# Performance work log

Measured on AMD Instinct MI355X. Metric: run time of the kernel, lower is better.

The kernel has to match this reference:

```python
import jax, jax.numpy as jnp
import numpy as np

NUM_QUANTIZERS = 8


def setup_inputs() -> dict:
    key = jax.random.key(0)
    k1, k2 = jax.random.split(key)
    B, W, C = 16, 2048, 512
    Q, K = NUM_QUANTIZERS, 1024
    x = jax.random.normal(k1, (B, W, C), dtype=jnp.float32)
    # per-stage codebooks (shared_codebook=False), xavier-normal-ish scale
    codebooks = jax.random.normal(k2, (Q, K, C), dtype=jnp.float32) * (2.0 / (K + C)) ** 0.5
    return {"x": x, "codebooks": codebooks}


def reference(x, codebooks):
    """Residual quantization: per-stage cdist+argmin+lookup+residual update.

    x: [B, W, C] encoder latents; codebooks: [Q, K, C].
    Returns (final_z_q [B*W, C], commitment_loss scalar) — final_z_q is
    sum over quantizer stages of the straight-through quantized outputs
    (is_train=True path).
    """
    B, W, C = x.shape
    first_z_e = x.reshape(B * W, C)            # (b w) c
    z_e = first_z_e
    z_d = jnp.zeros_like(first_z_e)
    quant_sum = jnp.zeros_like(first_z_e)
    q_latent = jnp.float32(0.0)
    e_latent = jnp.float32(0.0)
    rq_latent = jnp.float32(0.0)
    for i in range(codebooks.shape[0]):
        cb = codebooks[i]                      # [K, C]
        # squared euclidean distances (argmin-equivalent to torch.cdist)
        dist2 = (jnp.sum(z_e * z_e, axis=1, keepdims=True)
                 - 2.0 * (z_e @ cb.T)
                 + jnp.sum(cb * cb, axis=1))   # [N, K]
        idx = jnp.argmin(dist2, axis=1)        # [N]
        z_q = cb[idx]                          # codebook lookup, [N, C]
        z_d = z_d + jax.lax.stop_gradient(z_q)
        q_latent = q_latent + jnp.mean((jax.lax.stop_gradient(z_e) - z_q) ** 2)
        e_latent = e_latent + jnp.mean((z_e - jax.lax.stop_gradient(z_q)) ** 2)
        rq_latent = rq_latent + jnp.mean((first_z_e - z_d) ** 2)
        # straight-through estimator (is_train=True)
        z_q_st = z_e + jax.lax.stop_gradient(z_q - z_e)
        quant_sum = quant_sum + z_q_st
        z_e = z_e - z_q_st
    commitment_loss = 0.75 * q_latent + e_latent + rq_latent
    return quant_sum, commitment_loss
```

## Files before the change

kernel.cpp:

```cpp
#include <hip/hip_runtime.h>

#define N_ROWS 32768
#define C_DIM  512
#define K_CODES 1024
#define Q_STAGES 8

typedef __attribute__((ext_vector_type(8))) short bf16x8;
typedef __attribute__((ext_vector_type(4))) float f32x4;
typedef __attribute__((ext_vector_type(4))) unsigned short u16x4;
typedef __attribute__((ext_vector_type(8))) unsigned short u16x8;

#define ZEH_OFF 0ull
#define ZEL_OFF 33554432ull
#define CBH_OFF 67108864ull
#define CBL_OFF 68157440ull
#define C2_OFF  69206016ull
#define IDX_OFF 69238784ull
#define RPT_OFF 69304320ull

#define GLD(gp, lp) __builtin_amdgcn_global_load_lds( \
    (const __attribute__((address_space(1))) void*)(gp), \
    (__attribute__((address_space(3))) void*)(lp), 16, 0, 0)

__device__ __forceinline__ float bf_hi_f(float f) {
    return __uint_as_float(__float_as_uint(f) & 0xFFFF0000u);
}
__device__ __forceinline__ unsigned short bf_hi_u(float f) {
    return (unsigned short)(__float_as_uint(f) >> 16);
}
__device__ __forceinline__ float u2f(unsigned short u) {
    return __uint_as_float(((unsigned int)u) << 16);
}

__global__ __launch_bounds__(256) void split_kernel(
    const float* __restrict__ src, unsigned short* __restrict__ h,
    unsigned short* __restrict__ l, int n4)
{
    int i = blockIdx.x * 256 + threadIdx.x;
    if (i >= n4) return;
    float4 v = *(const float4*)(src + (size_t)i * 4);
    u16x4 hv, lv;
    float f, hf;
    f = v.x; hv[0] = bf_hi_u(f); hf = bf_hi_f(f); lv[0] = bf_hi_u(f - hf);
    f = v.y; hv[1] = bf_hi_u(f); hf = bf_hi_f(f); lv[1] = bf_hi_u(f - hf);
    f = v.z; hv[2] = bf_hi_u(f); hf = bf_hi_f(f); lv[2] = bf_hi_u(f - hf);
    f = v.w; hv[3] = bf_hi_u(f); hf = bf_hi_f(f); lv[3] = bf_hi_u(f - hf);
    *(u16x4*)(h + (size_t)i * 4) = hv;
    *(u16x4*)(l + (size_t)i * 4) = lv;
}

__global__ __launch_bounds__(256) void rowsq_kernel(
    const float* __restrict__ src, float* __restrict__ dst, int nrows)
{
    int wave = (blockIdx.x * blockDim.x + threadIdx.x) >> 6;
    int lane = threadIdx.x & 63;
    if (wave >= nrows) return;
    const float* p = src + (size_t)wave * C_DIM + lane * 8;
    float4 a = *(const float4*)p;
    float4 b = *(const float4*)(p + 4);
    float s = a.x*a.x + a.y*a.y + a.z*a.z + a.w*a.w
            + b.x*b.x + b.y*b.y + b.z*b.z + b.w*b.w;
    #pragma unroll
    for (int off = 1; off < 64; off <<= 1) s += __shfl_xor(s, off);
    if (lane == 0) dst[wave] = s;
}

#define DBM2 128
#define DBNC 256
#define DBK 32
#define NSTEPS 64

__global__ __launch_bounds__(512, 2) void dist_kernel(
    const unsigned short* __restrict__ zeh, const unsigned short* __restrict__ zel,
    const unsigned short* __restrict__ cbh, const unsigned short* __restrict__ cbl,
    const float* __restrict__ c2s, unsigned short* __restrict__ idx_out)
{
    __shared__ unsigned short sA[3][2][DBM2 * DBK];
    __shared__ unsigned short sB[3][2][DBNC * DBK];
    __shared__ float c2_lds[K_CODES];

    const int tid  = threadIdx.x;
    const int lane = tid & 63;
    const int w    = tid >> 6;
    const int wr   = w >> 2;
    const int wc   = w & 3;
    const int lr   = lane & 15;
    const int kg   = lane >> 4;
    const int row0 = blockIdx.x * DBM2;

    for (int i = tid; i < K_CODES; i += 512) c2_lds[i] = c2s[i];

    const int srow = lane >> 2;
    const int scol = (((lane & 3) ^ ((srow >> 1) & 3))) * 8;
    const int aslot = (kg ^ ((lr >> 1) & 3)) * 8;

    float rbv[4][4];
    int   rbi[4][4];
    #pragma unroll
    for (int i = 0; i < 4; ++i)
        #pragma unroll
        for (int r = 0; r < 4; ++r) { rbv[i][r] = 3.4e38f; rbi[i][r] = 0x7fffffff; }

    f32x4 acc[4][4];
    #pragma unroll
    for (int i = 0; i < 4; ++i)
        #pragma unroll
        for (int j = 0; j < 4; ++j) acc[i][j] = (f32x4)0.f;

    auto stage = [&](int t, int b) {
        const int col0 = (t >> 4) * DBNC;
        const int kk = (t & 15) * DBK;
        GLD(zeh + (size_t)(row0 + w * 16 + srow) * C_DIM + kk + scol,
            &sA[b][0][(w * 16) * DBK]);
        GLD(zel + (size_t)(row0 + w * 16 + srow) * C_DIM + kk + scol,
            &sA[b][1][(w * 16) * DBK]);
        #pragma unroll
        for (int u = 0; u < 2; ++u) {
            const int rB = w * 32 + u * 16;
            GLD(cbh + (size_t)(col0 + rB + srow) * C_DIM + kk + scol,
                &sB[b][0][rB * DBK]);
            GLD(cbl + (size_t)(col0 + rB + srow) * C_DIM + kk + scol,
                &sB[b][1][rB * DBK]);
        }
    };

    __syncthreads();
    stage(0, 0);
    stage(1, 1);
    asm volatile("s_waitcnt vmcnt(6)" ::: "memory");
    __builtin_amdgcn_s_barrier();

    bf16x8 ah[4], al[4], bh[4], bl[4];
    #pragma unroll
    for (int mi = 0; mi < 4; ++mi)
        ah[mi] = *(const bf16x8*)&sA[0][0][(wr * 64 + mi * 16 + lr) * DBK + aslot];
    #pragma unroll
    for (int ni = 0; ni < 4; ++ni)
        bh[ni] = *(const bf16x8*)&sB[0][0][(wc * 64 + ni * 16 + lr) * DBK + aslot];

    int cur = 0;
    #pragma unroll 1
    for (int t = 0; t < NSTEPS; ++t) {
        const int nxt = (cur == 2) ? 0 : cur + 1;
        const int n2  = (nxt == 2) ? 0 : nxt + 1;

        asm volatile("s_waitcnt lgkmcnt(0)" ::: "memory");
        __builtin_amdgcn_sched_barrier(0);
        #pragma unroll
        for (int ni = 0; ni < 4; ++ni)
            bl[ni] = *(const bf16x8*)&sB[cur][1][(wc * 64 + ni * 16 + lr) * DBK + aslot];
        __builtin_amdgcn_sched_barrier(0);
        __builtin_amdgcn_s_setprio(1);
        #pragma unroll
        for (int mi = 0; mi < 4; ++mi)
            #pragma unroll
            for (int ni = 0; ni < 4; ++ni)
                acc[mi][ni] = __builtin_amdgcn_mfma_f32_16x16x32_bf16(
                    ah[mi], bh[ni], acc[mi][ni], 0, 0, 0);
        __builtin_amdgcn_s_setprio(0);
        __builtin_amdgcn_sched_barrier(0);
        __builtin_amdgcn_s_barrier();

        asm volatile("s_waitcnt lgkmcnt(0)" ::: "memory");
        __builtin_amdgcn_sched_barrier(0);
        #pragma unroll
        for (int mi = 0; mi < 4; ++mi)
            al[mi] = *(const bf16x8*)&sA[cur][1][(wr * 64 + mi * 16 + lr) * DBK + aslot];
        if (t < NSTEPS - 2) stage(t + 2, n2);
        if (t <= NSTEPS - 3) {
            asm volatile("s_waitcnt vmcnt(6)" ::: "memory");
        } else {
            asm volatile("s_waitcnt vmcnt(0)" ::: "memory");
        }
        __builtin_amdgcn_sched_barrier(0);
        __builtin_amdgcn_s_setprio(1);
        #pragma unroll
        for (int mi = 0; mi < 4; ++mi)
            #pragma unroll
            for (int ni = 0; ni < 4; ++ni)
                acc[mi][ni] = __builtin_amdgcn_mfma_f32_16x16x32_bf16(
                    ah[mi], bl[ni], acc[mi][ni], 0, 0, 0);
        __builtin_amdgcn_s_setprio(0);
        __builtin_amdgcn_sched_barrier(0);
        __builtin_amdgcn_s_barrier();

        asm volatile("s_waitcnt lgkmcnt(0)" ::: "memory");
        __builtin_amdgcn_sched_barrier(0);
        __builtin_amdgcn_s_setprio(1);
        #pragma unroll
        for (int mi = 0; mi < 4; ++mi)
            #pragma unroll
            for (int ni = 0; ni < 4; ++ni)
                acc[mi][ni] = __builtin_amdgcn_mfma_f32_16x16x32_bf16(
                    al[mi], bh[ni], acc[mi][ni], 0, 0, 0);
        __builtin_amdgcn_s_setprio(0);
        __builtin_amdgcn_sched_barrier(0);
        if (t < NSTEPS - 1) {
            #pragma unroll
            for (int mi = 0; mi < 4; ++mi)
                ah[mi] = *(const bf16x8*)&sA[nxt][0][(wr * 64 + mi * 16 + lr) * DBK + aslot];
            #pragma unroll
            for (int ni = 0; ni < 4; ++ni)
                bh[ni] = *(const bf16x8*)&sB[nxt][0][(wc * 64 + ni * 16 + lr) * DBK + aslot];
        }
        if ((t & 15) == 15) {
            const int col0 = (t >> 4) * DBNC;
            #pragma unroll
            for (int ni = 0; ni < 4; ++ni) {
                const int code = col0 + wc * 64 + ni * 16 + lr;
                const float c2v = c2_lds[code];
                #pragma unroll
                for (int mi = 0; mi < 4; ++mi)
                    #pragma unroll
                    for (int r = 0; r < 4; ++r) {
                        float d = fmaf(-2.f, acc[mi][ni][r], c2v);
                        if (d < rbv[mi][r]) { rbv[mi][r] = d; rbi[mi][r] = code; }
                    }
            }
            #pragma unroll
            for (int i = 0; i < 4; ++i)
                #pragma unroll
                for (int j = 0; j < 4; ++j) acc[i][j] = (f32x4)0.f;
        }
        __builtin_amdgcn_s_barrier();
        cur = nxt;
    }

    #pragma unroll
    for (int off = 1; off < 16; off <<= 1) {
        #pragma unroll
        for (int mi = 0; mi < 4; ++mi)
            #pragma unroll
            for (int r = 0; r < 4; ++r) {
                float ov = __shfl_xor(rbv[mi][r], off);
                int   oi = __shfl_xor(rbi[mi][r], off);
                if (ov < rbv[mi][r] || (ov == rbv[mi][r] && oi < rbi[mi][r])) {
                    rbv[mi][r] = ov; rbi[mi][r] = oi;
                }
            }
    }

    __syncthreads();
    float (*s_v)[4] = (float (*)[4])&sA[0][0][0];
    int   (*s_i)[4] = (int (*)[4])((char*)&sA[0][0][0] + DBM2 * 4 * 4);
    if (lr == 0) {
        #pragma unroll
        for (int mi = 0; mi < 4; ++mi)
            #pragma unroll
            for (int r = 0; r < 4; ++r) {
                int lrow = wr * 64 + mi * 16 + kg * 4 + r;
                s_v[lrow][wc] = rbv[mi][r];
                s_i[lrow][wc] = rbi[mi][r];
            }
    }
    __syncthreads();
    if (tid < DBM2) {
        float bv = s_v[tid][0]; int bi = s_i[tid][0];
        #pragma unroll
        for (int c = 1; c < 4; ++c) {
            float v = s_v[tid][c]; int i = s_i[tid][c];
            if (v < bv || (v == bv && i < bi)) { bv = v; bi = i; }
        }
        idx_out[row0 + tid] = (unsigned short)bi;
    }
}

__global__ __launch_bounds__(1024) void update_kernel(
    const int s, const float* __restrict__ x, const float* __restrict__ cb,
    const float* __restrict__ cb_next, const unsigned short* __restrict__ idx_sel,
    float* __restrict__ out, unsigned short* __restrict__ zeh,
    unsigned short* __restrict__ zel, unsigned short* __restrict__ cbh,
    unsigned short* __restrict__ cbl, float* __restrict__ rpart)
{
    if (blockIdx.x >= 2048) {
        int i = (blockIdx.x - 2048) * 1024 + threadIdx.x;
        float4 v = *(const float4*)(cb_next + (size_t)i * 4);
        u16x4 hv, lv;
        float f, hf;
        f = v.x; hv[0] = bf_hi_u(f); hf = bf_hi_f(f); lv[0] = bf_hi_u(f - hf);
        f = v.y; hv[1] = bf_hi_u(f); hf = bf_hi_f(f); lv[1] = bf_hi_u(f - hf);
        f = v.z; hv[2] = bf_hi_u(f); hf = bf_hi_f(f); lv[2] = bf_hi_u(f - hf);
        f = v.w; hv[3] = bf_hi_u(f); hf = bf_hi_f(f); lv[3] = bf_hi_u(f - hf);
        *(u16x4*)(cbh + (size_t)i * 4) = hv;
        *(u16x4*)(cbl + (size_t)i * 4) = lv;
        return;
    }

    __shared__ float swsum[16];
    const int wid = threadIdx.x >> 6, lane = threadIdx.x & 63;
    const int r = blockIdx.x * 16 + wid;
    const int bi = idx_sel[r];
    const size_t base = (size_t)r * C_DIM + lane * 8;
    const float* q = cb + (size_t)bi * C_DIM + lane * 8;

    float4 q0 = *(const float4*)q;
    float4 q1 = *(const float4*)(q + 4);
    float qq[8] = {q0.x, q0.y, q0.z, q0.w, q1.x, q1.y, q1.z, q1.w};

    float v[8];
    if (s == 0) {
        float4 z0 = *(const float4*)(x + base);
        float4 z1 = *(const float4*)(x + base + 4);
        v[0]=z0.x; v[1]=z0.y; v[2]=z0.z; v[3]=z0.w;
        v[4]=z1.x; v[5]=z1.y; v[6]=z1.z; v[7]=z1.w;
    } else {
        u16x8 h = *(const u16x8*)(zeh + base);
        u16x8 l = *(const u16x8*)(zel + base);
        #pragma unroll
        for (int j = 0; j < 8; ++j) v[j] = u2f(h[j]) + u2f(l[j]);
    }

    float rr[8];
    #pragma unroll
    for (int j = 0; j < 8; ++j) rr[j] = v[j] - qq[j];

    if (s < Q_STAGES - 1) {
        u16x8 hh, ll;
        #pragma unroll
        for (int j = 0; j < 8; ++j) {
            hh[j] = bf_hi_u(rr[j]);
            float lo = rr[j] - bf_hi_f(rr[j]);
            ll[j] = bf_hi_u(lo);
        }
        *(u16x8*)(zeh + base) = hh;
        *(u16x8*)(zel + base) = ll;
    } else {
        float4 x0 = *(const float4*)(x + base);
        float4 x1 = *(const float4*)(x + base + 4);
        float4 o0, o1;
        o0.x = x0.x - rr[0]; o0.y = x0.y - rr[1];
        o0.z = x0.z - rr[2]; o0.w = x0.w - rr[3];
        o1.x = x1.x - rr[4]; o1.y = x1.y - rr[5];
        o1.z = x1.z - rr[6]; o1.w = x1.w - rr[7];
        *(float4*)(out + base)     = o0;
        *(float4*)(out + base + 4) = o1;
    }

    float ssum = 0.f;
    #pragma unroll
    for (int j = 0; j < 8; ++j) ssum += rr[j] * rr[j];
    #pragma unroll
    for (int off = 1; off < 64; off <<= 1) ssum += __shfl_xor(ssum, off);
    if (lane == 0) swsum[wid] = ssum;
    __syncthreads();
    if (threadIdx.x == 0) {
        float t = 0.f;
        #pragma unroll
        for (int i = 0; i < 16; ++i) t += swsum[i];
        rpart[blockIdx.x] = t;
    }
}

__global__ __launch_bounds__(1024) void finalize_all_kernel(
    const float* __restrict__ rpart, float* __restrict__ out_loss)
{
    __shared__ float sm[1024];
    const int t = threadIdx.x;
    float tot = 0.f;
    for (int s = 0; s < Q_STAGES; ++s) {
        sm[t] = rpart[s * 2048 + t] + rpart[s * 2048 + 1024 + t];
        __syncthreads();
        for (int w2 = 512; w2 > 0; w2 >>= 1) {
            if (t < w2) sm[t] += sm[t + w2];
            __syncthreads();
        }
        if (t == 0) tot += sm[0];
        __syncthreads();
    }
    if (t == 0) out_loss[0] = 2.75f * tot / (float)((size_t)N_ROWS * C_DIM);
}

extern "C" void kernel_launch(void* const* d_in, const int* in_sizes, int n_in,
                              void* d_out, int out_size, void* d_ws, size_t ws_size,
                              hipStream_t stream)
{
    const float* x   = (const float*)d_in[0];
    const float* cbs = (const float*)d_in[1];
    float* out = (float*)d_out;
    char* ws = (char*)d_ws;

    unsigned short* zeh = (unsigned short*)(ws + ZEH_OFF);
    unsigned short* zel = (unsigned short*)(ws + ZEL_OFF);
    unsigned short* cbh = (unsigned short*)(ws + CBH_OFF);
    unsigned short* cbl = (unsigned short*)(ws + CBL_OFF);
    float* c2    = (float*)(ws + C2_OFF);
    unsigned short* gidx = (unsigned short*)(ws + IDX_OFF);
    float* rpart = (float*)(ws + RPT_OFF);

    split_kernel<<<(N_ROWS * C_DIM / 4 + 255) / 256, 256, 0, stream>>>(
        x, zeh, zel, N_ROWS * C_DIM / 4);
    split_kernel<<<(K_CODES * C_DIM / 4 + 255) / 256, 256, 0, stream>>>(
        cbs, cbh, cbl, K_CODES * C_DIM / 4);
    rowsq_kernel<<<(Q_STAGES * K_CODES * 64) / 256, 256, 0, stream>>>(
        cbs, c2, Q_STAGES * K_CODES);

    for (int s = 0; s < Q_STAGES; ++s) {
        const float* cb  = cbs + (size_t)s * K_CODES * C_DIM;
        const float* cbn = (s < Q_STAGES - 1) ? cb + (size_t)K_CODES * C_DIM : cbs;
        dist_kernel<<<N_ROWS / DBM2, 512, 0, stream>>>(
            zeh, zel, cbh, cbl, c2 + (size_t)s * K_CODES, gidx);
        const int nblk = (s < Q_STAGES - 1) ? 2048 + 128 : 2048;
        update_kernel<<<nblk, 1024, 0, stream>>>(
            s, x, cb, cbn, gidx, out, zeh, zel, cbh, cbl, rpart + s * 2048);
    }
    finalize_all_kernel<<<1, 1024, 0, stream>>>(rpart, out + (size_t)N_ROWS * C_DIM);
}
```

Baseline: 1.184 ms.

## Simplify GEMM main loop to one barrier per k-step with upfront fragment loads

The finely interleaved schedule is replaced by a simpler one. Before, the loop had three barriers per step, pinned instruction ordering, and LDS fragment loads for the next step overlapped with the current MFMAs. Now each step waits for its stage, issues a single barrier, and loads all hi/lo A and B fragments from the current buffer. It then issues the global-to-LDS prefetch two steps ahead and runs all 48 MFMAs. This cuts barrier and scheduling overhead but exposes LDS read latency before each MFMA block, since fragments are no longer prefetched during compute.

```diff
diff --git a/kernel.cpp b/kernel.cpp
--- a/kernel.cpp
+++ b/kernel.cpp
@@ -127,29 +127,36 @@
     __syncthreads();
     stage(0, 0);
     stage(1, 1);
-    asm volatile("s_waitcnt vmcnt(6)" ::: "memory");
-    __builtin_amdgcn_s_barrier();
-
-    bf16x8 ah[4], al[4], bh[4], bl[4];
-    #pragma unroll
-    for (int mi = 0; mi < 4; ++mi)
-        ah[mi] = *(const bf16x8*)&sA[0][0][(wr * 64 + mi * 16 + lr) * DBK + aslot];
-    #pragma unroll
-    for (int ni = 0; ni < 4; ++ni)
-        bh[ni] = *(const bf16x8*)&sB[0][0][(wc * 64 + ni * 16 + lr) * DBK + aslot];
 
     int cur = 0;
     #pragma unroll 1
     for (int t = 0; t < NSTEPS; ++t) {
-        const int nxt = (cur == 2) ? 0 : cur + 1;
-        const int n2  = (nxt == 2) ? 0 : nxt + 1;
-
-        asm volatile("s_waitcnt lgkmcnt(0)" ::: "memory");
-        __builtin_amdgcn_sched_barrier(0);
-        #pragma unroll
-        for (int ni = 0; ni < 4; ++ni)
-            bl[ni] = *(const bf16x8*)&sB[cur][1][(wc * 64 + ni * 16 + lr) * DBK + aslot];
-        __builtin_amdgcn_sched_barrier(0);
+        if (t == NSTEPS - 1) {
+            asm volatile("s_waitcnt vmcnt(0)" ::: "memory");
+        } else {
+            asm volatile("s_waitcnt vmcnt(6)" ::: "memory");
+        }
+        __builtin_amdgcn_s_barrier();
+
+        bf16x8 ah[4], al[4], bh[4], bl[4];
+        #pragma unroll
+        for (int mi = 0; mi < 4; ++mi) {
+            const int rowoff = (wr * 64 + mi * 16 + lr) * DBK + aslot;
+            ah[mi] = *(const bf16x8*)&sA[cur][0][rowoff];
+            al[mi] = *(const bf16x8*)&sA[cur][1][rowoff];
+        }
+        #pragma unroll
+        for (int ni = 0; ni < 4; ++ni) {
+            const int rowoff = (wc * 64 + ni * 16 + lr) * DBK + aslot;
+            bh[ni] = *(const bf16x8*)&sB[cur][0][rowoff];
+            bl[ni] = *(const bf16x8*)&sB[cur][1][rowoff];
+        }
+
+        if (t < NSTEPS - 2) {
+            int nxt = cur + 2; if (nxt > 2) nxt -= 3;
+            stage(t + 2, nxt);
+        }
+
         __builtin_amdgcn_s_setprio(1);
         #pragma unroll
         for (int mi = 0; mi < 4; ++mi)
@@ -157,36 +164,12 @@
             for (int ni = 0; ni < 4; ++ni)
                 acc[mi][ni] = __builtin_amdgcn_mfma_f32_16x16x32_bf16(
                     ah[mi], bh[ni], acc[mi][ni], 0, 0, 0);
-        __builtin_amdgcn_s_setprio(0);
-        __builtin_amdgcn_sched_barrier(0);
-        __builtin_amdgcn_s_barrier();
-
-        asm volatile("s_waitcnt lgkmcnt(0)" ::: "memory");
-        __builtin_amdgcn_sched_barrier(0);
-        #pragma unroll
-        for (int mi = 0; mi < 4; ++mi)
-            al[mi] = *(const bf16x8*)&sA[cur][1][(wr * 64 + mi * 16 + lr) * DBK + aslot];
-        if (t < NSTEPS - 2) stage(t + 2, n2);
-        if (t <= NSTEPS - 3) {
-            asm volatile("s_waitcnt vmcnt(6)" ::: "memory");
-        } else {
-            asm volatile("s_waitcnt vmcnt(0)" ::: "memory");
-        }
-        __builtin_amdgcn_sched_barrier(0);
-        __builtin_amdgcn_s_setprio(1);
         #pragma unroll
         for (int mi = 0; mi < 4; ++mi)
             #pragma unroll
             for (int ni = 0; ni < 4; ++ni)
                 acc[mi][ni] = __builtin_amdgcn_mfma_f32_16x16x32_bf16(
                     ah[mi], bl[ni], acc[mi][ni], 0, 0, 0);
-        __builtin_amdgcn_s_setprio(0);
-        __builtin_amdgcn_sched_barrier(0);
-        __builtin_amdgcn_s_barrier();
-
-        asm volatile("s_waitcnt lgkmcnt(0)" ::: "memory");
-        __builtin_amdgcn_sched_barrier(0);
-        __builtin_amdgcn_s_setprio(1);
         #pragma unroll
         for (int mi = 0; mi < 4; ++mi)
             #pragma unroll
@@ -194,15 +177,7 @@
                 acc[mi][ni] = __builtin_amdgcn_mfma_f32_16x16x32_bf16(
                     al[mi], bh[ni], acc[mi][ni], 0, 0, 0);
         __builtin_amdgcn_s_setprio(0);
-        __builtin_amdgcn_sched_barrier(0);
-        if (t < NSTEPS - 1) {
-            #pragma unroll
-            for (int mi = 0; mi < 4; ++mi)
-                ah[mi] = *(const bf16x8*)&sA[nxt][0][(wr * 64 + mi * 16 + lr) * DBK + aslot];
-            #pragma unroll
-            for (int ni = 0; ni < 4; ++ni)
-                bh[ni] = *(const bf16x8*)&sB[nxt][0][(wc * 64 + ni * 16 + lr) * DBK + aslot];
-        }
+
         if ((t & 15) == 15) {
             const int col0 = (t >> 4) * DBNC;
             #pragma unroll
@@ -222,8 +197,8 @@
                 #pragma unroll
                 for (int j = 0; j < 4; ++j) acc[i][j] = (f32x4)0.f;
         }
-        __builtin_amdgcn_s_barrier();
-        cur = nxt;
+
+        cur = (cur == 2) ? 0 : cur + 1;
     }
 
     #pragma unroll
```

Result: faster. 988.2 us (-16.6%).
